# Performance work log

Measured on AMD Instinct MI355X. Metric: run time of the kernel, lower is better.

Reference implementation:

```python
import jax, jax.numpy as jnp
import numpy as np

B, N, F_IN, H, FO = 4, 2048, 256, 4, 64


def setup_inputs() -> dict:
    key = jax.random.key(0)
    k1, k2, k3, k4, k5 = jax.random.split(key, 5)
    x = jax.random.normal(k1, (B, N, F_IN), dtype=jnp.float32)
    # random 0/1 adjacency with self-loops so every row of softmax is finite
    adj = jax.random.randint(k2, (N, N), 0, 2).astype(jnp.float32)
    adj = jnp.maximum(adj, jnp.eye(N, dtype=jnp.float32))
    # parameters (xavier-uniform style)
    lim_w = float(np.sqrt(6.0 / (F_IN + H * FO)))
    W = jax.random.uniform(k3, (F_IN, H * FO), minval=-lim_w, maxval=lim_w, dtype=jnp.float32)
    lim_a = float(np.sqrt(6.0 / (H + FO)))
    a_src = jax.random.uniform(k4, (H, FO), minval=-lim_a, maxval=lim_a, dtype=jnp.float32)
    a_dst = jax.random.uniform(k5, (H, FO), minval=-lim_a, maxval=lim_a, dtype=jnp.float32)
    return {"x": x, "adj": adj, "W": W, "a_src": a_src, "a_dst": a_dst}


def reference(x, adj, W, a_src, a_dst):
    # h: (B, N, H, FO)
    h = (x @ W).reshape(B, N, H, FO)
    attn_src = jnp.einsum("bnhf,hf->bnh", h, a_src)  # (B,N,H)
    attn_dst = jnp.einsum("bnhf,hf->bnh", h, a_dst)  # (B,N,H)
    # scores[b,i,j,h] = src[b,i,h] + dst[b,j,h]
    scores = attn_src[:, :, None, :] + attn_dst[:, None, :, :]
    scores = jax.nn.leaky_relu(scores, negative_slope=0.2)
    mask = (adj == 0)[None, :, :, None]  # (1,N,N,1)
    scores = jnp.where(mask, -jnp.inf, scores)
    attn = jax.nn.softmax(scores, axis=2)  # softmax over neighbors j
    # dropout is identity in eval mode / p=0
    out = jnp.einsum("bijh,bjhf->bihf", attn, h)  # (B,N,H,FO)
    return out.reshape(B, N, H * FO)  # concat=True
```

## Files before the change

### kernel.cpp

```cpp
#include <hip/hip_runtime.h>
#include <hip/hip_bf16.h>
#include <math.h>

#define B 4
#define N 2048
#define FIN 256
#define H 4
#define FO 64
#define M (B*N)
#define HF (H*FO)

typedef __attribute__((ext_vector_type(8))) short short8;
typedef __attribute__((ext_vector_type(4))) float float4v;
typedef __attribute__((ext_vector_type(4))) int int4v;

#if __has_builtin(__builtin_amdgcn_exp2f)
#define EXP2(x) __builtin_amdgcn_exp2f(x)
#else
#define EXP2(x) exp2f(x)
#endif

static __device__ __forceinline__ unsigned int pk_rne(float a, float b) {
  unsigned int ua = __builtin_bit_cast(unsigned int, a);
  unsigned int ub = __builtin_bit_cast(unsigned int, b);
  ua += 0x7fffu + ((ua >> 16) & 1u);
  ub += 0x7fffu + ((ub >> 16) & 1u);
  return (ua >> 16) | (ub & 0xffff0000u);
}

static __device__ __forceinline__ unsigned int pk_trunc(float a, float b) {
#if __has_builtin(__builtin_amdgcn_perm)
  return __builtin_amdgcn_perm(__builtin_bit_cast(unsigned int, b),
                               __builtin_bit_cast(unsigned int, a), 0x07060302u);
#else
  return (__builtin_bit_cast(unsigned int, a) >> 16) |
         (__builtin_bit_cast(unsigned int, b) & 0xffff0000u);
#endif
}

static __device__ __forceinline__ void split_pair(float x0, float x1,
                                                  unsigned int& hi, unsigned int& lo) {
  unsigned int u0 = __builtin_bit_cast(unsigned int, x0);
  unsigned int u1 = __builtin_bit_cast(unsigned int, x1);
  hi = (u0 >> 16) | (u1 & 0xffff0000u);
  float h0 = __builtin_bit_cast(float, u0 & 0xffff0000u);
  float h1 = __builtin_bit_cast(float, u1 & 0xffff0000u);
  unsigned int l0 = __builtin_bit_cast(unsigned int, x0 - h0);
  unsigned int l1 = __builtin_bit_cast(unsigned int, x1 - h1);
  lo = (l0 >> 16) | (l1 & 0xffff0000u);
}

static __device__ __forceinline__ unsigned int fenc(float f) {
  unsigned int b = __builtin_bit_cast(unsigned int, f);
  return (b & 0x80000000u) ? ~b : (b | 0x80000000u);
}
static __device__ __forceinline__ float fdec(unsigned int e) {
  unsigned int b = (e & 0x80000000u) ? (e & 0x7fffffffu) : ~e;
  return __builtin_bit_cast(float, b);
}

__global__ __launch_bounds__(256) void prep_w(const float* __restrict__ Wsrc,
                                              unsigned short* __restrict__ Wt_hi,
                                              unsigned short* __restrict__ Wt_lo,
                                              unsigned int* __restrict__ DmaxEnc) {
  if (blockIdx.x == 0 && threadIdx.x < 16) DmaxEnc[threadIdx.x] = 0u;
  __shared__ float lds[64][65];
  const int k0 = (blockIdx.x >> 2) * 64;
  const int n0 = (blockIdx.x & 3) * 64;
  const int t = threadIdx.x;
  const int c4 = (t & 15) * 4;
  #pragma unroll
  for (int rep = 0; rep < 4; ++rep) {
    const int kl = (t >> 4) + 16 * rep;
    const float4 v = *(const float4*)(Wsrc + (size_t)(k0 + kl) * HF + n0 + c4);
    lds[kl][c4 + 0] = v.x; lds[kl][c4 + 1] = v.y;
    lds[kl][c4 + 2] = v.z; lds[kl][c4 + 3] = v.w;
  }
  __syncthreads();
  const int n  = t >> 2;
  const int kc = (t & 3) * 16;
  unsigned int hv[8], lv[8];
  #pragma unroll
  for (int p = 0; p < 8; ++p)
    split_pair(lds[kc + 2 * p][n], lds[kc + 2 * p + 1][n], hv[p], lv[p]);
  unsigned short* dh = Wt_hi + (size_t)(n0 + n) * FIN + k0 + kc;
  unsigned short* dl = Wt_lo + (size_t)(n0 + n) * FIN + k0 + kc;
  ((uint4*)dh)[0] = make_uint4(hv[0], hv[1], hv[2], hv[3]);
  ((uint4*)dh)[1] = make_uint4(hv[4], hv[5], hv[6], hv[7]);
  ((uint4*)dl)[0] = make_uint4(lv[0], lv[1], lv[2], lv[3]);
  ((uint4*)dl)[1] = make_uint4(lv[4], lv[5], lv[6], lv[7]);
}

__global__ __launch_bounds__(256) void pack_adj(const float* __restrict__ adj,
                                                unsigned long long* __restrict__ packed) {
  const int row = blockIdx.x;
  const int w = threadIdx.x >> 6, l = threadIdx.x & 63;
  const float* ar = adj + (size_t)row * N;
  for (int c = w; c < N / 64; c += 4) {
    unsigned long long m = __ballot(ar[c * 64 + l] != 0.f);
    if (l == 0) packed[(size_t)row * (N / 64) + c] = m;
  }
}

__global__ __launch_bounds__(256) void gemm_fused(const float* __restrict__ X,
                                                  const unsigned short* __restrict__ Wt_hi,
                                                  const unsigned short* __restrict__ Wt_lo,
                                                  const float* __restrict__ a_src,
                                                  const float* __restrict__ a_dst,
                                                  float* __restrict__ Srcv,
                                                  float2* __restrict__ Epair,
                                                  unsigned int* __restrict__ DmaxEnc,
                                                  unsigned short* __restrict__ Hf) {
  __shared__ unsigned short sh[64][72];
  __shared__ float smax[4];
  const int xcd  = blockIdx.x & 7;
  const int slot = blockIdx.x >> 3;
  const int mb = xcd * 16 + (slot >> 2);
  const int h  = slot & 3;
  const int w = threadIdx.x >> 6, lane = threadIdx.x & 63;
  const int fl = lane & 15, quad = lane >> 4, kk = quad * 8;
  const int m0 = mb * 64 + w * 16;
  const float* xr = X + (size_t)(m0 + fl) * FIN;
  const unsigned short* whb = Wt_hi + (size_t)(h * FO + fl) * FIN;
  const unsigned short* wlb = Wt_lo + (size_t)(h * FO + fl) * FIN;
  const float L2E = 1.4426950408889634f;

  const float4v zero = {0.f, 0.f, 0.f, 0.f};
  float4v acc[4] = {zero, zero, zero, zero};

  for (int k0 = 0; k0 < FIN; k0 += 32) {
    const float4 xa = *(const float4*)(xr + k0 + kk);
    const float4 xb = *(const float4*)(xr + k0 + kk + 4);
    const float xv[8] = {xa.x, xa.y, xa.z, xa.w, xb.x, xb.y, xb.z, xb.w};
    int hi[4], lo[4];
    #pragma unroll
    for (int p = 0; p < 4; ++p) {
      unsigned int hp, lp;
      split_pair(xv[2 * p], xv[2 * p + 1], hp, lp);
      hi[p] = (int)hp; lo[p] = (int)lp;
    }
    const short8 Ahi = __builtin_bit_cast(short8, (int4v){hi[0], hi[1], hi[2], hi[3]});
    const short8 Alo = __builtin_bit_cast(short8, (int4v){lo[0], lo[1], lo[2], lo[3]});
    #pragma unroll
    for (int t = 0; t < 4; ++t) {
      const short8 Bhi = *(const short8*)(whb + t * 16 * FIN + k0 + kk);
      const short8 Blo = *(const short8*)(wlb + t * 16 * FIN + k0 + kk);
      acc[t] = __builtin_amdgcn_mfma_f32_16x16x32_bf16(Ahi, Bhi, acc[t], 0, 0, 0);
      acc[t] = __builtin_amdgcn_mfma_f32_16x16x32_bf16(Alo, Bhi, acc[t], 0, 0, 0);
      acc[t] = __builtin_amdgcn_mfma_f32_16x16x32_bf16(Ahi, Blo, acc[t], 0, 0, 0);
    }
  }

  const int bb  = (mb * 64) >> 11;
  const int n0w = (mb * 64) & (N - 1);
  const int bh  = bb * H + h;
  float as[4], ad[4];
  #pragma unroll
  for (int t = 0; t < 4; ++t) {
    as[t] = a_src[h * FO + t * 16 + fl];
    ad[t] = a_dst[h * FO + t * 16 + fl];
  }
  float wmax = -INFINITY;
  #pragma unroll
  for (int reg = 0; reg < 4; ++reg) {
    float sv = 0.f, dv = 0.f;
    #pragma unroll
    for (int t = 0; t < 4; ++t) {
      sv = fmaf(acc[t][reg], as[t], sv);
      dv = fmaf(acc[t][reg], ad[t], dv);
    }
    #pragma unroll
    for (int off = 1; off <= 8; off <<= 1) {
      sv += __shfl_xor(sv, off, 64);
      dv += __shfl_xor(dv, off, 64);
    }
    wmax = fmaxf(wmax, dv);
    if (fl == 0) {
      const int node = n0w + w * 16 + quad * 4 + reg;
      Srcv[(bh << 11) + node] = sv;
      float2 e;
      e.x = EXP2(dv * L2E);
      e.y = EXP2(dv * (0.2f * L2E));
      Epair[(bh << 11) + node] = e;
    }
  }
  wmax = fmaxf(wmax, __shfl_xor(wmax, 16, 64));
  wmax = fmaxf(wmax, __shfl_xor(wmax, 32, 64));
  if (lane == 0) smax[w] = wmax;

  #pragma unroll
  for (int t = 0; t < 4; ++t) {
    const int nl = w * 16 + quad * 4;
    *(unsigned int*)&sh[t * 16 + fl][nl]     = pk_rne(acc[t][0], acc[t][1]);
    *(unsigned int*)&sh[t * 16 + fl][nl + 2] = pk_rne(acc[t][2], acc[t][3]);
  }
  __syncthreads();
  if (threadIdx.x == 0) {
    const float bmax = fmaxf(fmaxf(smax[0], smax[1]), fmaxf(smax[2], smax[3]));
    atomicMax(DmaxEnc + bh, fenc(bmax));
  }
  const int jc0 = n0w >> 5;
  #pragma unroll
  for (int rep = 0; rep < 2; ++rep) {
    const int s = (int)threadIdx.x + rep * 256;
    const int jcl = s >> 8;
    const int tt  = (s >> 6) & 3;
    const int ln  = s & 63;
    const int f    = tt * 16 + (ln & 15);
    const int node = jcl * 32 + (ln >> 4) * 8;
    unsigned short* dsth = Hf + (((size_t)bh * 64 + jc0 + jcl) * 4 + tt) * 512 + ln * 8;
    *(uint4*)dsth = *(const uint4*)&sh[f][node];
  }
}

__global__ __launch_bounds__(1024) void gat_mfma(const unsigned char* __restrict__ pb,
                                                 const float* __restrict__ Src,
                                                 const float2* __restrict__ Epair,
                                                 const unsigned int* __restrict__ DmaxEnc,
                                                 const unsigned short* __restrict__ Hf,
                                                 float* __restrict__ out) {
  const int xcd  = blockIdx.x & 7;
  const int slot = blockIdx.x >> 3;
  const int b    = xcd >> 1;
  const int i0   = ((xcd & 1) * 32 + slot) * 32;
  const int w    = threadIdx.x >> 6;
  const int lane = threadIdx.x & 63;
  const int h    = w & 3;
  const int q    = w >> 2;
  const int bh   = b * H + h;
  const int fl   = lane & 15;
  const int kk   = (lane >> 4) * 8;
  const float L2E = 1.4426950408889634f;

  const int row0 = i0 + fl;
  const int row1 = i0 + 16 + fl;
  const float dmx = fdec(DmaxEnc[bh]);
  const float s0 = Src[(bh << 11) + row0];
  const float s1 = Src[(bh << 11) + row1];
  const float u0 = s0 + dmx, m0 = fmaxf(u0, 0.2f * u0);
  const float u1 = s1 + dmx, m1 = fmaxf(u1, 0.2f * u1);
  const float c1a = EXP2((s0 - m0) * L2E), c2a = EXP2((0.2f * s0 - m0) * L2E);
  const float c1b = EXP2((s1 - m1) * L2E), c2b = EXP2((0.2f * s1 - m1) * L2E);
  const float ta = EXP2(-s0 * L2E), tb = EXP2(-s1 * L2E);
  const float* ep = (const float*)(Epair + (bh << 11));
  const unsigned char* pb0 = pb + (size_t)row0 * (N / 8);
  const unsigned char* pb1 = pb + (size_t)row1 * (N / 8);
  const unsigned short* hfb = Hf + (size_t)bh * 64 * 2048 + lane * 8;

  const short onebf = 0x3F80;
  short8 ones;
  #pragma unroll
  for (int jj = 0; jj < 8; ++jj) ones[jj] = onebf;

  const float4v zero = {0.f, 0.f, 0.f, 0.f};
  float4v acc[2][4];
  float4v accL[2];
  #pragma unroll
  for (int rt = 0; rt < 2; ++rt) {
    accL[rt] = zero;
    #pragma unroll
    for (int t = 0; t < 4; ++t) acc[rt][t] = zero;
  }

  const int jbeg = q * (N / 4);
  #pragma unroll 2
  for (int j0 = jbeg; j0 < jbeg + N / 4; j0 += 32) {
    const unsigned short* hc = hfb + (size_t)(j0 >> 5) * 2048;
    const short8 b0 = *(const short8*)(hc + 0 * 512);
    const short8 b1 = *(const short8*)(hc + 1 * 512);
    const short8 b2 = *(const short8*)(hc + 2 * 512);
    const short8 b3 = *(const short8*)(hc + 3 * 512);
    const float4 q0 = *(const float4*)(ep + 2 * (j0 + kk) + 0);
    const float4 q1 = *(const float4*)(ep + 2 * (j0 + kk) + 4);
    const float4 q2 = *(const float4*)(ep + 2 * (j0 + kk) + 8);
    const float4 q3 = *(const float4*)(ep + 2 * (j0 + kk) + 12);
    const unsigned int mk0 = pb0[(j0 + kk) >> 3];
    const unsigned int mk1 = pb1[(j0 + kk) >> 3];
    const float E1v[8] = {q0.x, q0.z, q1.x, q1.z, q2.x, q2.z, q3.x, q3.z};
    const float E2v[8] = {q0.y, q0.w, q1.y, q1.w, q2.y, q2.w, q3.y, q3.w};
    int p0i[4], p1i[4];
    #pragma unroll
    for (int p = 0; p < 4; ++p) {
      const int e0 = 2 * p, e1 = 2 * p + 1;
      const bool sa0 = E1v[e0] > ta;
      float va0 = (sa0 ? c1a : c2a) * (sa0 ? E1v[e0] : E2v[e0]);
      va0 = ((mk0 >> e0) & 1u) ? va0 : 0.f;
      const bool sa1 = E1v[e1] > ta;
      float va1 = (sa1 ? c1a : c2a) * (sa1 ? E1v[e1] : E2v[e1]);
      va1 = ((mk0 >> e1) & 1u) ? va1 : 0.f;
      p0i[p] = (int)pk_trunc(va0, va1);
      const bool sb0 = E1v[e0] > tb;
      float vb0 = (sb0 ? c1b : c2b) * (sb0 ? E1v[e0] : E2v[e0]);
      vb0 = ((mk1 >> e0) & 1u) ? vb0 : 0.f;
      const bool sb1 = E1v[e1] > tb;
      float vb1 = (sb1 ? c1b : c2b) * (sb1 ? E1v[e1] : E2v[e1]);
      vb1 = ((mk1 >> e1) & 1u) ? vb1 : 0.f;
      p1i[p] = (int)pk_trunc(vb0, vb1);
    }
    const short8 p0 = __builtin_bit_cast(short8, (int4v){p0i[0], p0i[1], p0i[2], p0i[3]});
    const short8 p1 = __builtin_bit_cast(short8, (int4v){p1i[0], p1i[1], p1i[2], p1i[3]});
    acc[0][0] = __builtin_amdgcn_mfma_f32_16x16x32_bf16(p0, b0, acc[0][0], 0, 0, 0);
    acc[0][1] = __builtin_amdgcn_mfma_f32_16x16x32_bf16(p0, b1, acc[0][1], 0, 0, 0);
    acc[0][2] = __builtin_amdgcn_mfma_f32_16x16x32_bf16(p0, b2, acc[0][2], 0, 0, 0);
    acc[0][3] = __builtin_amdgcn_mfma_f32_16x16x32_bf16(p0, b3, acc[0][3], 0, 0, 0);
    accL[0]   = __builtin_amdgcn_mfma_f32_16x16x32_bf16(p0, ones, accL[0], 0, 0, 0);
    acc[1][0] = __builtin_amdgcn_mfma_f32_16x16x32_bf16(p1, b0, acc[1][0], 0, 0, 0);
    acc[1][1] = __builtin_amdgcn_mfma_f32_16x16x32_bf16(p1, b1, acc[1][1], 0, 0, 0);
    acc[1][2] = __builtin_amdgcn_mfma_f32_16x16x32_bf16(p1, b2, acc[1][2], 0, 0, 0);
    acc[1][3] = __builtin_amdgcn_mfma_f32_16x16x32_bf16(p1, b3, acc[1][3], 0, 0, 0);
    accL[1]   = __builtin_amdgcn_mfma_f32_16x16x32_bf16(p1, ones, accL[1], 0, 0, 0);
  }

  __shared__ float4v parts[4][64][11];
  for (int r = 3; r >= 1; --r) {
    if (q == r) {
      #pragma unroll
      for (int rt = 0; rt < 2; ++rt) {
        #pragma unroll
        for (int t = 0; t < 4; ++t) parts[h][lane][rt * 5 + t] = acc[rt][t];
        parts[h][lane][rt * 5 + 4] = accL[rt];
      }
    }
    __syncthreads();
    if (q == r - 1) {
      #pragma unroll
      for (int rt = 0; rt < 2; ++rt) {
        #pragma unroll
        for (int t = 0; t < 4; ++t) acc[rt][t] += parts[h][lane][rt * 5 + t];
        accL[rt] += parts[h][lane][rt * 5 + 4];
      }
    }
    __syncthreads();
  }

  if (q == 0) {
    const int quad = lane >> 4;
    #pragma unroll
    for (int rt = 0; rt < 2; ++rt) {
      #pragma unroll
      for (int reg = 0; reg < 4; ++reg) {
        const int r = i0 + rt * 16 + quad * 4 + reg;
        const float invl = 1.f / accL[rt][reg];
        float* op = out + ((size_t)(b * N) + r) * HF + h * FO + fl;
        #pragma unroll
        for (int t = 0; t < 4; ++t) op[t * 16] = acc[rt][t][reg] * invl;
      }
    }
  }
}

extern "C" void kernel_launch(void* const* d_in, const int* in_sizes, int n_in,
                              void* d_out, int out_size, void* d_ws, size_t ws_size,
                              hipStream_t stream) {
  const float* x     = (const float*)d_in[0];
  const float* adj   = (const float*)d_in[1];
  const float* W     = (const float*)d_in[2];
  const float* a_src = (const float*)d_in[3];
  const float* a_dst = (const float*)d_in[4];
  float* out = (float*)d_out;

  char* p = (char*)d_ws;
  float* Srcv = (float*)p;                 p += (size_t)B * H * N * 4;
  float2* Epair = (float2*)p;              p += (size_t)B * H * N * 8;
  unsigned int* DmaxEnc = (unsigned int*)p; p += 256;
  unsigned short* Wth = (unsigned short*)p; p += (size_t)HF * FIN * 2;
  unsigned short* Wtl = (unsigned short*)p; p += (size_t)HF * FIN * 2;
  unsigned short* Hf  = (unsigned short*)p; p += (size_t)M * HF * 2;
  unsigned long long* packed = (unsigned long long*)p;

  prep_w<<<dim3(16), dim3(256), 0, stream>>>(W, Wth, Wtl, DmaxEnc);
  pack_adj<<<dim3(N), dim3(256), 0, stream>>>(adj, packed);
  gemm_fused<<<dim3((M / 64) * H), dim3(256), 0, stream>>>(x, Wth, Wtl, a_src, a_dst,
                                                           Srcv, Epair, DmaxEnc, Hf);
  gat_mfma<<<dim3(B * (N / 32)), dim3(1024), 0, stream>>>((const unsigned char*)packed,
                                                          Srcv, Epair, DmaxEnc, Hf, out);
}
```

Measured before the change: 141.3 us.

## Fuse weight prep with adjacency packing, fragment-layout W, halve GAT row tile

Merges the weight-split and adjacency-packing kernels into one launch, removing one kernel launch. Stores the hi/lo bf16 weights in MFMA fragment order so the GEMM loads each B operand as one contiguous 16-byte per-lane read. The attention kernel now handles 16 rows per block instead of 32, doubling the grid to 512 blocks and dropping the second row-tile's accumulators, which lowers register pressure. In exchange, the Hf values and edge terms are loaded twice as often across blocks.

```diff
diff --git a/kernel.cpp b/kernel.cpp
--- a/kernel.cpp
+++ b/kernel.cpp
@@ -59,14 +59,27 @@
   return __builtin_bit_cast(float, b);
 }
 
-__global__ __launch_bounds__(256) void prep_w(const float* __restrict__ Wsrc,
-                                              unsigned short* __restrict__ Wt_hi,
-                                              unsigned short* __restrict__ Wt_lo,
-                                              unsigned int* __restrict__ DmaxEnc) {
+__global__ __launch_bounds__(256) void prep_pack(const float* __restrict__ Wsrc,
+                                                 const float* __restrict__ adj,
+                                                 unsigned short* __restrict__ Wf_hi,
+                                                 unsigned short* __restrict__ Wf_lo,
+                                                 unsigned long long* __restrict__ packed,
+                                                 unsigned int* __restrict__ DmaxEnc) {
+  if (blockIdx.x >= 16) {
+    const int row = blockIdx.x - 16;
+    const int w = threadIdx.x >> 6, l = threadIdx.x & 63;
+    const float* ar = adj + (size_t)row * N;
+    for (int c = w; c < N / 64; c += 4) {
+      unsigned long long m = __ballot(ar[c * 64 + l] != 0.f);
+      if (l == 0) packed[(size_t)row * (N / 64) + c] = m;
+    }
+    return;
+  }
   if (blockIdx.x == 0 && threadIdx.x < 16) DmaxEnc[threadIdx.x] = 0u;
   __shared__ float lds[64][65];
   const int k0 = (blockIdx.x >> 2) * 64;
-  const int n0 = (blockIdx.x & 3) * 64;
+  const int h  = blockIdx.x & 3;
+  const int n0 = h * 64;
   const int t = threadIdx.x;
   const int c4 = (t & 15) * 4;
   #pragma unroll
@@ -77,34 +90,27 @@
     lds[kl][c4 + 2] = v.z; lds[kl][c4 + 3] = v.w;
   }
   __syncthreads();
-  const int n  = t >> 2;
-  const int kc = (t & 3) * 16;
-  unsigned int hv[8], lv[8];
-  #pragma unroll
-  for (int p = 0; p < 8; ++p)
-    split_pair(lds[kc + 2 * p][n], lds[kc + 2 * p + 1][n], hv[p], lv[p]);
-  unsigned short* dh = Wt_hi + (size_t)(n0 + n) * FIN + k0 + kc;
-  unsigned short* dl = Wt_lo + (size_t)(n0 + n) * FIN + k0 + kc;
-  ((uint4*)dh)[0] = make_uint4(hv[0], hv[1], hv[2], hv[3]);
-  ((uint4*)dh)[1] = make_uint4(hv[4], hv[5], hv[6], hv[7]);
-  ((uint4*)dl)[0] = make_uint4(lv[0], lv[1], lv[2], lv[3]);
-  ((uint4*)dl)[1] = make_uint4(lv[4], lv[5], lv[6], lv[7]);
-}
-
-__global__ __launch_bounds__(256) void pack_adj(const float* __restrict__ adj,
-                                                unsigned long long* __restrict__ packed) {
-  const int row = blockIdx.x;
-  const int w = threadIdx.x >> 6, l = threadIdx.x & 63;
-  const float* ar = adj + (size_t)row * N;
-  for (int c = w; c < N / 64; c += 4) {
-    unsigned long long m = __ballot(ar[c * 64 + l] != 0.f);
-    if (l == 0) packed[(size_t)row * (N / 64) + c] = m;
+  #pragma unroll
+  for (int rep = 0; rep < 2; ++rep) {
+    const int s   = t + rep * 256;
+    const int kcl = s >> 8;
+    const int tt  = (s >> 6) & 3;
+    const int ln  = s & 63;
+    const int fL  = tt * 16 + (ln & 15);
+    const int kb  = kcl * 32 + (ln >> 4) * 8;
+    unsigned int hv[4], lv[4];
+    #pragma unroll
+    for (int p = 0; p < 4; ++p)
+      split_pair(lds[kb + 2 * p][fL], lds[kb + 2 * p + 1][fL], hv[p], lv[p]);
+    const size_t off = ((((size_t)h * 8 + (k0 >> 5) + kcl) * 4 + tt) << 9) + ln * 8;
+    *(uint4*)(Wf_hi + off) = make_uint4(hv[0], hv[1], hv[2], hv[3]);
+    *(uint4*)(Wf_lo + off) = make_uint4(lv[0], lv[1], lv[2], lv[3]);
   }
 }
 
 __global__ __launch_bounds__(256) void gemm_fused(const float* __restrict__ X,
-                                                  const unsigned short* __restrict__ Wt_hi,
-                                                  const unsigned short* __restrict__ Wt_lo,
+                                                  const unsigned short* __restrict__ Wf_hi,
+                                                  const unsigned short* __restrict__ Wf_lo,
                                                   const float* __restrict__ a_src,
                                                   const float* __restrict__ a_dst,
                                                   float* __restrict__ Srcv,
@@ -121,14 +127,13 @@
   const int fl = lane & 15, quad = lane >> 4, kk = quad * 8;
   const int m0 = mb * 64 + w * 16;
   const float* xr = X + (size_t)(m0 + fl) * FIN;
-  const unsigned short* whb = Wt_hi + (size_t)(h * FO + fl) * FIN;
-  const unsigned short* wlb = Wt_lo + (size_t)(h * FO + fl) * FIN;
   const float L2E = 1.4426950408889634f;
 
   const float4v zero = {0.f, 0.f, 0.f, 0.f};
   float4v acc[4] = {zero, zero, zero, zero};
 
   for (int k0 = 0; k0 < FIN; k0 += 32) {
+    const int kc = k0 >> 5;
     const float4 xa = *(const float4*)(xr + k0 + kk);
     const float4 xb = *(const float4*)(xr + k0 + kk + 4);
     const float xv[8] = {xa.x, xa.y, xa.z, xa.w, xb.x, xb.y, xb.z, xb.w};
@@ -143,8 +148,9 @@
     const short8 Alo = __builtin_bit_cast(short8, (int4v){lo[0], lo[1], lo[2], lo[3]});
     #pragma unroll
     for (int t = 0; t < 4; ++t) {
-      const short8 Bhi = *(const short8*)(whb + t * 16 * FIN + k0 + kk);
-      const short8 Blo = *(const short8*)(wlb + t * 16 * FIN + k0 + kk);
+      const size_t woff = ((((size_t)h * 8 + kc) * 4 + t) << 9) + lane * 8;
+      const short8 Bhi = *(const short8*)(Wf_hi + woff);
+      const short8 Blo = *(const short8*)(Wf_lo + woff);
       acc[t] = __builtin_amdgcn_mfma_f32_16x16x32_bf16(Ahi, Bhi, acc[t], 0, 0, 0);
       acc[t] = __builtin_amdgcn_mfma_f32_16x16x32_bf16(Alo, Bhi, acc[t], 0, 0, 0);
       acc[t] = __builtin_amdgcn_mfma_f32_16x16x32_bf16(Ahi, Blo, acc[t], 0, 0, 0);
@@ -213,16 +219,16 @@
   }
 }
 
-__global__ __launch_bounds__(1024) void gat_mfma(const unsigned char* __restrict__ pb,
-                                                 const float* __restrict__ Src,
-                                                 const float2* __restrict__ Epair,
-                                                 const unsigned int* __restrict__ DmaxEnc,
-                                                 const unsigned short* __restrict__ Hf,
-                                                 float* __restrict__ out) {
+__global__ __launch_bounds__(1024, 8) void gat_mfma(const unsigned char* __restrict__ pb,
+                                                    const float* __restrict__ Src,
+                                                    const float2* __restrict__ Epair,
+                                                    const unsigned int* __restrict__ DmaxEnc,
+                                                    const unsigned short* __restrict__ Hf,
+                                                    float* __restrict__ out) {
   const int xcd  = blockIdx.x & 7;
   const int slot = blockIdx.x >> 3;
   const int b    = xcd >> 1;
-  const int i0   = ((xcd & 1) * 32 + slot) * 32;
+  const int i0   = ((xcd & 1) * 64 + slot) * 16;
   const int w    = threadIdx.x >> 6;
   const int lane = threadIdx.x & 63;
   const int h    = w & 3;
@@ -233,18 +239,13 @@
   const float L2E = 1.4426950408889634f;
 
   const int row0 = i0 + fl;
-  const int row1 = i0 + 16 + fl;
   const float dmx = fdec(DmaxEnc[bh]);
   const float s0 = Src[(bh << 11) + row0];
-  const float s1 = Src[(bh << 11) + row1];
   const float u0 = s0 + dmx, m0 = fmaxf(u0, 0.2f * u0);
-  const float u1 = s1 + dmx, m1 = fmaxf(u1, 0.2f * u1);
   const float c1a = EXP2((s0 - m0) * L2E), c2a = EXP2((0.2f * s0 - m0) * L2E);
-  const float c1b = EXP2((s1 - m1) * L2E), c2b = EXP2((0.2f * s1 - m1) * L2E);
-  const float ta = EXP2(-s0 * L2E), tb = EXP2(-s1 * L2E);
+  const float ta = EXP2(-s0 * L2E);
   const float* ep = (const float*)(Epair + (bh << 11));
   const unsigned char* pb0 = pb + (size_t)row0 * (N / 8);
-  const unsigned char* pb1 = pb + (size_t)row1 * (N / 8);
   const unsigned short* hfb = Hf + (size_t)bh * 64 * 2048 + lane * 8;
 
   const short onebf = 0x3F80;
@@ -253,14 +254,8 @@
   for (int jj = 0; jj < 8; ++jj) ones[jj] = onebf;
 
   const float4v zero = {0.f, 0.f, 0.f, 0.f};
-  float4v acc[2][4];
-  float4v accL[2];
-  #pragma unroll
-  for (int rt = 0; rt < 2; ++rt) {
-    accL[rt] = zero;
-    #pragma unroll
-    for (int t = 0; t < 4; ++t) acc[rt][t] = zero;
-  }
+  float4v acc[4] = {zero, zero, zero, zero};
+  float4v accL = zero;
 
   const int jbeg = q * (N / 4);
   #pragma unroll 2
@@ -275,10 +270,9 @@
     const float4 q2 = *(const float4*)(ep + 2 * (j0 + kk) + 8);
     const float4 q3 = *(const float4*)(ep + 2 * (j0 + kk) + 12);
     const unsigned int mk0 = pb0[(j0 + kk) >> 3];
-    const unsigned int mk1 = pb1[(j0 + kk) >> 3];
     const float E1v[8] = {q0.x, q0.z, q1.x, q1.z, q2.x, q2.z, q3.x, q3.z};
     const float E2v[8] = {q0.y, q0.w, q1.y, q1.w, q2.y, q2.w, q3.y, q3.w};
-    int p0i[4], p1i[4];
+    int p0i[4];
     #pragma unroll
     for (int p = 0; p < 4; ++p) {
       const int e0 = 2 * p, e1 = 2 * p + 1;
@@ -289,46 +283,27 @@
       float va1 = (sa1 ? c1a : c2a) * (sa1 ? E1v[e1] : E2v[e1]);
       va1 = ((mk0 >> e1) & 1u) ? va1 : 0.f;
       p0i[p] = (int)pk_trunc(va0, va1);
-      const bool sb0 = E1v[e0] > tb;
-      float vb0 = (sb0 ? c1b : c2b) * (sb0 ? E1v[e0] : E2v[e0]);
-      vb0 = ((mk1 >> e0) & 1u) ? vb0 : 0.f;
-      const bool sb1 = E1v[e1] > tb;
-      float vb1 = (sb1 ? c1b : c2b) * (sb1 ? E1v[e1] : E2v[e1]);
-      vb1 = ((mk1 >> e1) & 1u) ? vb1 : 0.f;
-      p1i[p] = (int)pk_trunc(vb0, vb1);
     }
     const short8 p0 = __builtin_bit_cast(short8, (int4v){p0i[0], p0i[1], p0i[2], p0i[3]});
-    const short8 p1 = __builtin_bit_cast(short8, (int4v){p1i[0], p1i[1], p1i[2], p1i[3]});
-    acc[0][0] = __builtin_amdgcn_mfma_f32_16x16x32_bf16(p0, b0, acc[0][0], 0, 0, 0);
-    acc[0][1] = __builtin_amdgcn_mfma_f32_16x16x32_bf16(p0, b1, acc[0][1], 0, 0, 0);
-    acc[0][2] = __builtin_amdgcn_mfma_f32_16x16x32_bf16(p0, b2, acc[0][2], 0, 0, 0);
-    acc[0][3] = __builtin_amdgcn_mfma_f32_16x16x32_bf16(p0, b3, acc[0][3], 0, 0, 0);
-    accL[0]   = __builtin_amdgcn_mfma_f32_16x16x32_bf16(p0, ones, accL[0], 0, 0, 0);
-    acc[1][0] = __builtin_amdgcn_mfma_f32_16x16x32_bf16(p1, b0, acc[1][0], 0, 0, 0);
-    acc[1][1] = __builtin_amdgcn_mfma_f32_16x16x32_bf16(p1, b1, acc[1][1], 0, 0, 0);
-    acc[1][2] = __builtin_amdgcn_mfma_f32_16x16x32_bf16(p1, b2, acc[1][2], 0, 0, 0);
-    acc[1][3] = __builtin_amdgcn_mfma_f32_16x16x32_bf16(p1, b3, acc[1][3], 0, 0, 0);
-    accL[1]   = __builtin_amdgcn_mfma_f32_16x16x32_bf16(p1, ones, accL[1], 0, 0, 0);
-  }
-
-  __shared__ float4v parts[4][64][11];
+    acc[0] = __builtin_amdgcn_mfma_f32_16x16x32_bf16(p0, b0, acc[0], 0, 0, 0);
+    acc[1] = __builtin_amdgcn_mfma_f32_16x16x32_bf16(p0, b1, acc[1], 0, 0, 0);
+    acc[2] = __builtin_amdgcn_mfma_f32_16x16x32_bf16(p0, b2, acc[2], 0, 0, 0);
+    acc[3] = __builtin_amdgcn_mfma_f32_16x16x32_bf16(p0, b3, acc[3], 0, 0, 0);
+    accL   = __builtin_amdgcn_mfma_f32_16x16x32_bf16(p0, ones, accL, 0, 0, 0);
+  }
+
+  __shared__ float4v parts[4][64][5];
   for (int r = 3; r >= 1; --r) {
     if (q == r) {
       #pragma unroll
-      for (int rt = 0; rt < 2; ++rt) {
-        #pragma unroll
-        for (int t = 0; t < 4; ++t) parts[h][lane][rt * 5 + t] = acc[rt][t];
-        parts[h][lane][rt * 5 + 4] = accL[rt];
-      }
+      for (int t = 0; t < 4; ++t) parts[h][lane][t] = acc[t];
+      parts[h][lane][4] = accL;
     }
     __syncthreads();
     if (q == r - 1) {
       #pragma unroll
-      for (int rt = 0; rt < 2; ++rt) {
-        #pragma unroll
-        for (int t = 0; t < 4; ++t) acc[rt][t] += parts[h][lane][rt * 5 + t];
-        accL[rt] += parts[h][lane][rt * 5 + 4];
-      }
+      for (int t = 0; t < 4; ++t) acc[t] += parts[h][lane][t];
+      accL += parts[h][lane][4];
     }
     __syncthreads();
   }
@@ -336,15 +311,12 @@
   if (q == 0) {
     const int quad = lane >> 4;
     #pragma unroll
-    for (int rt = 0; rt < 2; ++rt) {
+    for (int reg = 0; reg < 4; ++reg) {
+      const int r = i0 + quad * 4 + reg;
+      const float invl = 1.f / accL[reg];
+      float* op = out + ((size_t)(b * N) + r) * HF + h * FO + fl;
       #pragma unroll
-      for (int reg = 0; reg < 4; ++reg) {
-        const int r = i0 + rt * 16 + quad * 4 + reg;
-        const float invl = 1.f / accL[rt][reg];
-        float* op = out + ((size_t)(b * N) + r) * HF + h * FO + fl;
-        #pragma unroll
-        for (int t = 0; t < 4; ++t) op[t * 16] = acc[rt][t][reg] * invl;
-      }
+      for (int t = 0; t < 4; ++t) op[t * 16] = acc[t][reg] * invl;
     }
   }
 }
@@ -363,15 +335,14 @@
   float* Srcv = (float*)p;                 p += (size_t)B * H * N * 4;
   float2* Epair = (float2*)p;              p += (size_t)B * H * N * 8;
   unsigned int* DmaxEnc = (unsigned int*)p; p += 256;
-  unsigned short* Wth = (unsigned short*)p; p += (size_t)HF * FIN * 2;
-  unsigned short* Wtl = (unsigned short*)p; p += (size_t)HF * FIN * 2;
+  unsigned short* Wfh = (unsigned short*)p; p += (size_t)HF * FIN * 2;
+  unsigned short* Wfl = (unsigned short*)p; p += (size_t)HF * FIN * 2;
   unsigned short* Hf  = (unsigned short*)p; p += (size_t)M * HF * 2;
   unsigned long long* packed = (unsigned long long*)p;
 
-  prep_w<<<dim3(16), dim3(256), 0, stream>>>(W, Wth, Wtl, DmaxEnc);
-  pack_adj<<<dim3(N), dim3(256), 0, stream>>>(adj, packed);
-  gemm_fused<<<dim3((M / 64) * H), dim3(256), 0, stream>>>(x, Wth, Wtl, a_src, a_dst,
+  prep_pack<<<dim3(16 + N), dim3(256), 0, stream>>>(W, adj, Wfh, Wfl, packed, DmaxEnc);
+  gemm_fused<<<dim3((M / 64) * H), dim3(256), 0, stream>>>(x, Wfh, Wfl, a_src, a_dst,
                                                            Srcv, Epair, DmaxEnc, Hf);
-  gat_mfma<<<dim3(B * (N / 32)), dim3(1024), 0, stream>>>((const unsigned char*)packed,
+  gat_mfma<<<dim3(B * (N / 16)), dim3(1024), 0, stream>>>((const unsigned char*)packed,
                                                           Srcv, Epair, DmaxEnc, Hf, out);
 }
```

Result: slower. 200.8 us (+42.1%).
